# Optimization experiments

Measured on AMD Instinct MI355X. Metric: run time of the kernel, lower is better.

## Reference

```python
import jax, jax.numpy as jnp
import numpy as np

N = 1048576
C = 128
EPS = 1e-12


def setup_inputs() -> dict:
    key = jax.random.key(0)
    k1, k2 = jax.random.split(key)
    y_pred = jax.random.normal(k1, (N, C), dtype=jnp.float32)
    y_true = jax.random.randint(k2, (N,), 0, C, dtype=jnp.int64)
    return {"y_pred": y_pred, "y_true": y_true}


def reference(y_pred, y_true):
    # confusion matrix via scatter-add: rows = true class, cols = predicted class
    pred = jnp.argmax(y_pred, axis=1)
    conf = jnp.zeros((C, C), dtype=jnp.int32).at[y_true, pred].add(1)
    conf_f = conf.astype(jnp.float32)

    TP = jnp.diagonal(conf_f)  # [C]
    # Faithful to the original torch code: idx is a LONG tensor of ones with a 0
    # at position c, used as a gather index (not a boolean mask). Hence:
    #   FP_c = sum_j conf[c, idx[j]] = (C-1)*conf[c,1] + conf[c,0]
    #   FN_c = sum_j conf[idx[j], c] = (C-1)*conf[1,c] + conf[0,c]
    FP = (C - 1) * conf_f[:, 1] + conf_f[:, 0]
    FN = (C - 1) * conf_f[1, :] + conf_f[0, :]

    sensitivity = TP / (TP + FN + EPS)
    precision = TP / (TP + FP + EPS)
    f1 = 2.0 * (precision * sensitivity / (precision + sensitivity + EPS))
    return jnp.mean(f1)
```

## Files before the change

kernel.cpp:

```cpp
#include <hip/hip_runtime.h>

#define NROWS 1048576
#define NC    128
#define EPSF  1e-12f

__global__ void __launch_bounds__(256) argmax_conf_kernel(
    const float* __restrict__ y_pred,
    const int*   __restrict__ y_true,
    int*         __restrict__ conf,
    int n_rows)
{
    const int tid     = blockIdx.x * blockDim.x + threadIdx.x;
    const int lane    = threadIdx.x & 63;
    const int q       = lane & 15;
    const int quarter = (lane >> 4);
    const int wave    = tid >> 6;
    const int nwaves  = (gridDim.x * blockDim.x) >> 6;

    for (int base = wave * 4; base < n_rows; base += nwaves * 4) {
        const int row = base + quarter;

        float v   = -3.4e38f;
        int   idx = 0;

        if (row < n_rows) {
            const float4* rowp = (const float4*)(y_pred + (size_t)row * NC);
            const float4 a = rowp[q];
            const float4 b = rowp[q + 16];

            v = a.x; idx = 4 * q;
            if (a.y > v) { v = a.y; idx = 4 * q + 1; }
            if (a.z > v) { v = a.z; idx = 4 * q + 2; }
            if (a.w > v) { v = a.w; idx = 4 * q + 3; }
            if (b.x > v) { v = b.x; idx = 64 + 4 * q; }
            if (b.y > v) { v = b.y; idx = 64 + 4 * q + 1; }
            if (b.z > v) { v = b.z; idx = 64 + 4 * q + 2; }
            if (b.w > v) { v = b.w; idx = 64 + 4 * q + 3; }
        }

        #pragma unroll
        for (int off = 1; off < 16; off <<= 1) {
            float ov = __shfl_xor(v, off, 64);
            int   oi = __shfl_xor(idx, off, 64);
            if (ov > v || (ov == v && oi < idx)) { v = ov; idx = oi; }
        }

        if (q == 0 && row < n_rows) {
            const int t = y_true[row];
            atomicAdd(&conf[t * NC + idx], 1);
        }
    }
}

__global__ void f1_mean_kernel(const int* __restrict__ conf,
                               float* __restrict__ out)
{
    __shared__ float partial[NC];
    const int c = threadIdx.x;

    const float TP = (float)conf[c * NC + c];
    const float FP = (float)(NC - 1) * (float)conf[c * NC + 1] + (float)conf[c * NC + 0];
    const float FN = (float)(NC - 1) * (float)conf[1 * NC + c] + (float)conf[0 * NC + c];

    const float sens = TP / (TP + FN + EPSF);
    const float prec = TP / (TP + FP + EPSF);
    const float f1   = 2.0f * (prec * sens / (prec + sens + EPSF));

    partial[c] = f1;
    __syncthreads();

    #pragma unroll
    for (int s = 64; s > 0; s >>= 1) {
        if (c < s) partial[c] += partial[c + s];
        __syncthreads();
    }

    if (c == 0) out[0] = partial[0] / (float)NC;
}

extern "C" void kernel_launch(void* const* d_in, const int* in_sizes, int n_in,
                              void* d_out, int out_size, void* d_ws, size_t ws_size,
                              hipStream_t stream)
{
    const float* y_pred = (const float*)d_in[0];
    const int*   y_true = (const int*)d_in[1];
    float*       out    = (float*)d_out;
    int*         conf   = (int*)d_ws;

    const int n_rows = in_sizes[1];

    hipMemsetAsync(conf, 0, NC * NC * sizeof(int), stream);

    argmax_conf_kernel<<<2048, 256, 0, stream>>>(y_pred, y_true, conf, n_rows);

    f1_mean_kernel<<<1, NC, 0, stream>>>(conf, out);
}
```

Measured before the change: 682.4 us.

## Accumulate only needed confusion entries in shared-memory privatized counters

The full 128x128 confusion matrix is no longer built. Only the entries the F1 formula reads are counted: the diagonal, columns 0 and 1, and rows 0 and 1. Each block keeps these 640 counters in shared memory with LDS atomics and flushes non-zero values to global memory once at the end. This removes about a million contended global atomics and shrinks the memset, at the cost of a few branches per row and a flush pass per block. The y_true load is also issued before the row loads so its latency overlaps with them.

```diff
diff --git a/kernel.cpp b/kernel.cpp
--- a/kernel.cpp
+++ b/kernel.cpp
@@ -4,12 +4,24 @@
 #define NC    128
 #define EPSF  1e-12f
 
+#define DIAG  0
+#define COL0  (NC)
+#define COL1  (2 * NC)
+#define ROW0  (3 * NC)
+#define ROW1  (4 * NC)
+#define NCOUNT (5 * NC)
+
 __global__ void __launch_bounds__(256) argmax_conf_kernel(
     const float* __restrict__ y_pred,
     const int*   __restrict__ y_true,
-    int*         __restrict__ conf,
+    int*         __restrict__ counts,
     int n_rows)
 {
+    __shared__ int lcnt[NCOUNT];
+
+    for (int i = threadIdx.x; i < NCOUNT; i += blockDim.x) lcnt[i] = 0;
+    __syncthreads();
+
     const int tid     = blockIdx.x * blockDim.x + threadIdx.x;
     const int lane    = threadIdx.x & 63;
     const int q       = lane & 15;
@@ -22,6 +34,8 @@
 
         float v   = -3.4e38f;
         int   idx = 0;
+
+        const int t = (q == 0 && row < n_rows) ? y_true[row] : 0;
 
         if (row < n_rows) {
             const float4* rowp = (const float4*)(y_pred + (size_t)row * NC);
@@ -46,21 +60,31 @@
         }
 
         if (q == 0 && row < n_rows) {
-            const int t = y_true[row];
-            atomicAdd(&conf[t * NC + idx], 1);
+            if (idx == t) atomicAdd(&lcnt[DIAG + t], 1);
+            if (idx == 0) atomicAdd(&lcnt[COL0 + t], 1);
+            if (idx == 1) atomicAdd(&lcnt[COL1 + t], 1);
+            if (t == 0)   atomicAdd(&lcnt[ROW0 + idx], 1);
+            if (t == 1)   atomicAdd(&lcnt[ROW1 + idx], 1);
         }
+    }
+
+    __syncthreads();
+
+    for (int i = threadIdx.x; i < NCOUNT; i += blockDim.x) {
+        const int c = lcnt[i];
+        if (c) atomicAdd(&counts[i], c);
     }
 }
 
-__global__ void f1_mean_kernel(const int* __restrict__ conf,
+__global__ void f1_mean_kernel(const int* __restrict__ counts,
                                float* __restrict__ out)
 {
     __shared__ float partial[NC];
     const int c = threadIdx.x;
 
-    const float TP = (float)conf[c * NC + c];
-    const float FP = (float)(NC - 1) * (float)conf[c * NC + 1] + (float)conf[c * NC + 0];
-    const float FN = (float)(NC - 1) * (float)conf[1 * NC + c] + (float)conf[0 * NC + c];
+    const float TP = (float)counts[DIAG + c];
+    const float FP = (float)(NC - 1) * (float)counts[COL1 + c] + (float)counts[COL0 + c];
+    const float FN = (float)(NC - 1) * (float)counts[ROW1 + c] + (float)counts[ROW0 + c];
 
     const float sens = TP / (TP + FN + EPSF);
     const float prec = TP / (TP + FP + EPSF);
@@ -85,13 +109,13 @@
     const float* y_pred = (const float*)d_in[0];
     const int*   y_true = (const int*)d_in[1];
     float*       out    = (float*)d_out;
-    int*         conf   = (int*)d_ws;
+    int*         counts = (int*)d_ws;
 
     const int n_rows = in_sizes[1];
 
-    hipMemsetAsync(conf, 0, NC * NC * sizeof(int), stream);
+    hipMemsetAsync(counts, 0, NCOUNT * sizeof(int), stream);
 
-    argmax_conf_kernel<<<2048, 256, 0, stream>>>(y_pred, y_true, conf, n_rows);
+    argmax_conf_kernel<<<2048, 256, 0, stream>>>(y_pred, y_true, counts, n_rows);
 
-    f1_mean_kernel<<<1, NC, 0, stream>>>(conf, out);
+    f1_mean_kernel<<<1, NC, 0, stream>>>(counts, out);
 }
```

New measurement: 680.2 us. About the same (-0.3%).
